# Optimization experiments

Hardware: AMD Instinct MI355X
Metric: run time of the kernel (lower is better)

## Reference

```python
import jax, jax.numpy as jnp
import numpy as np

V = 27      # vocab (26 upper chars + 1)
E = 64      # embedding dim
H = 100     # GRU hidden dim
S = 10      # sequence length
B = 32768   # batch


def setup_inputs() -> dict:
    key = jax.random.key(0)
    ks = jax.random.split(key, 10)
    s = 0.08
    return {
        "encoder_X": jax.random.randint(ks[0], (B, S), 0, V),
        "decoder_X": jax.random.randint(ks[1], (B, S), 0, V),
        "emb": jax.random.normal(ks[2], (V, E)) * s,
        "enc_Wih": jax.random.normal(ks[3], (3 * H, E)) * s,
        "enc_Whh": jax.random.normal(ks[4], (3 * H, H)) * s,
        "enc_bih": jnp.zeros((3 * H,)),
        "enc_bhh": jnp.zeros((3 * H,)),
        "dec_Wih": jax.random.normal(ks[5], (3 * H, E + H)) * s,
        "dec_Whh": jax.random.normal(ks[6], (3 * H, H)) * s,
        "dec_bih": jnp.zeros((3 * H,)),
        "dec_bhh": jnp.zeros((3 * H,)),
        "attn_W": jax.random.normal(ks[7], (H, H)) * s,
        "lin_W": jax.random.normal(ks[8], (V, H)) * s,
        "lin_b": jnp.zeros((V,)),
    }


def gru_cell(x, h, Wih, Whh, bih, bhh):
    # PyTorch GRU cell: gates ordered [reset, update, new]
    gx = x @ Wih.T + bih            # [B, 3H]
    gh = h @ Whh.T + bhh            # [B, 3H]
    xr, xz, xn = jnp.split(gx, 3, axis=-1)
    hr, hz, hn = jnp.split(gh, 3, axis=-1)
    r = jax.nn.sigmoid(xr + hr)
    z = jax.nn.sigmoid(xz + hz)
    n = jnp.tanh(xn + r * hn)
    return (1.0 - z) * n + z * h


def reference(encoder_X, decoder_X, emb, enc_Wih, enc_Whh, enc_bih, enc_bhh,
              dec_Wih, dec_Whh, dec_bih, dec_bhh, attn_W, lin_W, lin_b):
    b = encoder_X.shape[0]
    # ---- encoder ----
    enc_e = emb[encoder_X]                         # [B, S, E]
    h0 = jnp.zeros((b, H), dtype=emb.dtype)

    def enc_step(h, x_t):
        h2 = gru_cell(x_t, h, enc_Wih, enc_Whh, enc_bih, enc_bhh)
        return h2, h2

    hT, enc_seq = jax.lax.scan(enc_step, h0, jnp.swapaxes(enc_e, 0, 1))
    enc_out = jnp.swapaxes(enc_seq, 0, 1)          # [B, S, H]

    # attention_W(encoder_out) is step-invariant: precompute once
    We = enc_out @ attn_W.T                        # [B, S, H]

    # ---- decoder with per-step bilinear attention ----
    dec_e = emb[decoder_X]                         # [B, S, E]

    def dec_step(h, x_t):
        score = jnp.einsum('bsh,bh->bs', We, h)    # [B, S]
        w = jax.nn.softmax(score, axis=1)
        ctx = jnp.einsum('bs,bsh->bh', w, enc_out) # [B, H]
        inp = jnp.concatenate([x_t, ctx], axis=-1) # [B, E+H]
        h2 = gru_cell(inp, h, dec_Wih, dec_Whh, dec_bih, dec_bhh)
        return h2, h2

    _, dec_seq = jax.lax.scan(dec_step, hT, jnp.swapaxes(dec_e, 0, 1))
    dec_out = jnp.swapaxes(dec_seq, 0, 1)          # [B, S, H]

    logits = dec_out @ lin_W.T + lin_b             # [B, S, V]
    return logits.reshape(-1, V)                   # [B*S, V]
```

## Files before the change

kernel.cpp:

```cpp
#include <hip/hip_runtime.h>
#include <hip/hip_bf16.h>

typedef short s16x8 __attribute__((ext_vector_type(8)));
typedef float f32x4 __attribute__((ext_vector_type(4)));
typedef unsigned short ushort_t;
typedef unsigned int uint;

#define DEV static __device__ __forceinline__

namespace {
constexpr int kV = 27, kS = 10, kB = 32768;
constexpr int BT = 32, NB = kB / BT;

constexpr size_t O_BE_R   = 0;
constexpr size_t O_BE_Z   = O_BE_R   + (size_t)7*4*512;
constexpr size_t O_BE_NH  = O_BE_Z   + (size_t)7*4*512;
constexpr size_t O_BE_NHL = O_BE_NH  + (size_t)7*4*512;
constexpr size_t O_BE_NX  = O_BE_NHL + (size_t)7*4*512;
constexpr size_t O_BE_NXL = O_BE_NX  + (size_t)7*1*512;
constexpr size_t O_BD_R   = O_BE_NXL + (size_t)7*1*512;
constexpr size_t O_BD_Z   = O_BD_R   + (size_t)7*8*512;
constexpr size_t O_BD_NC  = O_BD_Z   + (size_t)7*8*512;
constexpr size_t O_BD_NCL = O_BD_NC  + (size_t)7*5*512;
constexpr size_t O_BD_NH  = O_BD_NCL + (size_t)7*5*512;
constexpr size_t O_BD_NHL = O_BD_NH  + (size_t)7*4*512;
constexpr size_t O_WATT   = O_BD_NHL + (size_t)7*4*512;
constexpr size_t O_BLIN   = O_WATT   + (size_t)7*4*512;
constexpr size_t O_BLINL  = O_BLIN   + (size_t)2*4*512;

constexpr int ESTR = 102;
constexpr int EPL  = BT * ESTR;
}

DEV float sigm(float x) { return 1.f / (1.f + __expf(-x)); }
DEV float tanh_(float x) {
  const float ax = fabsf(x), t = __expf(-2.f * ax);
  return copysignf((1.f - t) / (1.f + t), x);
}
DEV ushort_t f2b(float f) { return __builtin_bit_cast(ushort_t, __float2bfloat16(f)); }
DEV float b2f(ushort_t u) { return __builtin_bit_cast(float, (uint)u << 16); }
DEV float lo16(uint u) { return __builtin_bit_cast(float, u << 16); }
DEV float hi16(uint u) { return __builtin_bit_cast(float, u & 0xFFFF0000u); }
DEV f32x4 MF(s16x8 a, s16x8 b, f32x4 c) {
  return __builtin_amdgcn_mfma_f32_16x16x32_bf16(a, b, c, 0, 0, 0);
}
DEV float dot64(const float* __restrict__ a, const float* __restrict__ b) {
  float s = 0.f;
#pragma unroll 16
  for (int k = 0; k < 64; ++k) s += a[k] * b[k];
  return s;
}
DEV void storeHL(ushort_t* ws, size_t offH, size_t offL, int e, float v) {
  const ushort_t h = f2b(v);
  ws[offH + e] = h;
  ws[offL + e] = f2b(v - b2f(h));
}

DEV s16x8 ldBF(const ushort_t* p, int fragIdx, int lane) {
  return __builtin_bit_cast(s16x8, *(const uint4*)(p + ((size_t)fragIdx << 9) + (lane << 3)));
}
DEV uint swzb(int row, int byteoff) { return (uint)((row * 512 + byteoff) ^ ((row & 7) << 4)); }
DEV s16x8 ldA(const ushort_t* A, int rt, int kf, int cl, int g4) {
  const int row = rt * 16 + cl;
  return __builtin_bit_cast(s16x8, *(const uint4*)((const char*)A + swzb(row, kf * 64 + g4 * 16)));
}
DEV void stA16(ushort_t* A, int row, int col, ushort_t v) {
  *(ushort_t*)((char*)A + swzb(row, col * 2)) = v;
}
DEV void stA32(ushort_t* A, int row, int byteoff, uint v) {
  *(uint*)((char*)A + swzb(row, byteoff)) = v;
}
DEV uint ldA32(const ushort_t* A, int row, int byteoff) {
  return *(const uint*)((const char*)A + swzb(row, byteoff));
}

__global__ void seq2seq_setup(const float* __restrict__ emb,
    const float* __restrict__ eWih, const float* __restrict__ eWhh,
    const float* __restrict__ ebih, const float* __restrict__ ebhh,
    const float* __restrict__ dWih, const float* __restrict__ dWhh,
    const float* __restrict__ dbih, const float* __restrict__ dbhh,
    const float* __restrict__ attnW, const float* __restrict__ linW,
    const float* __restrict__ linb, ushort_t* __restrict__ ws) {
  const int t0 = blockIdx.x * blockDim.x + threadIdx.x;
  const int stp = gridDim.x * blockDim.x;

  for (int e = t0; e < 7 * 4 * 512; e += stp) {
    int c = e >> 11, rem = e & 2047, fi = rem >> 9, l = (rem >> 3) & 63, i8 = rem & 7;
    int d = 16 * c + (l & 15);
    int k = fi * 32 + ((l >> 4) << 3) + i8;
    float vr = 0, vz = 0, vnh = 0;
    if (d < 100) {
      if (k < 100) { vr = eWhh[d*100+k]; vz = eWhh[(100+d)*100+k]; vnh = eWhh[(200+d)*100+k]; }
      else if (k < 127) {
        int tok = k - 100;
        vr = dot64(emb + tok*64, eWih + (size_t)d*64);
        vz = dot64(emb + tok*64, eWih + (size_t)(100+d)*64);
      } else {
        vr = ebih[d] + ebhh[d]; vz = ebih[100+d] + ebhh[100+d]; vnh = ebhh[200+d];
      }
    }
    ws[O_BE_R + e] = f2b(vr);
    ws[O_BE_Z + e] = f2b(vz);
    storeHL(ws, O_BE_NH, O_BE_NHL, e, vnh);
  }
  for (int e = t0; e < 7 * 512; e += stp) {
    int c = e >> 9, l = (e >> 3) & 63, i8 = e & 7;
    int d = 16 * c + (l & 15);
    int k = 96 + ((l >> 4) << 3) + i8;
    float v = 0;
    if (d < 100) {
      if (k >= 100 && k < 127) v = dot64(emb + (k-100)*64, eWih + (size_t)(200+d)*64);
      else if (k == 127) v = ebih[200+d];
    }
    storeHL(ws, O_BE_NX, O_BE_NXL, e, v);
  }
  for (int e = t0; e < 7 * 8 * 512; e += stp) {
    int c = e >> 12, rem = e & 4095, fi = rem >> 9, l = (rem >> 3) & 63, i8 = rem & 7;
    int d = 16 * c + (l & 15);
    int k = fi * 32 + ((l >> 4) << 3) + i8;
    float vr = 0, vz = 0;
    if (d < 100) {
      int wr = d, wz = 100 + d;
      if (k < 100)       { vr = dWih[(size_t)wr*164+64+k]; vz = dWih[(size_t)wz*164+64+k]; }
      else if (k < 128)  { }
      else if (k < 228)  { vr = dWhh[wr*100+k-128];        vz = dWhh[wz*100+k-128]; }
      else if (k < 255)  { vr = dot64(emb+(k-228)*64, dWih+(size_t)wr*164);
                           vz = dot64(emb+(k-228)*64, dWih+(size_t)wz*164); }
      else               { vr = dbih[wr]+dbhh[wr];         vz = dbih[wz]+dbhh[wz]; }
    }
    ws[O_BD_R + e] = f2b(vr);
    ws[O_BD_Z + e] = f2b(vz);
  }
  for (int e = t0; e < 7 * 5 * 512; e += stp) {
    int c = e / (5*512), rem = e - c*5*512, fi = rem >> 9, l = (rem >> 3) & 63, i8 = rem & 7;
    int fid = (fi < 4) ? fi : 7;
    int d = 16 * c + (l & 15);
    int k = fid * 32 + ((l >> 4) << 3) + i8;
    float v = 0;
    if (d < 100) {
      int wr = 200 + d;
      if (k < 100) v = dWih[(size_t)wr*164+64+k];
      else if (k >= 228 && k < 255) v = dot64(emb+(k-228)*64, dWih+(size_t)wr*164);
      else if (k == 255) v = dbih[wr];
    }
    storeHL(ws, O_BD_NC, O_BD_NCL, e, v);
  }
  for (int e = t0; e < 7 * 4 * 512; e += stp) {
    int c = e >> 11, rem = e & 2047, fi = rem >> 9, l = (rem >> 3) & 63, i8 = rem & 7;
    int d = 16 * c + (l & 15);
    int k = (4 + fi) * 32 + ((l >> 4) << 3) + i8;
    float v = 0;
    if (d < 100) {
      int wr = 200 + d;
      if (k >= 128 && k < 228) v = dWhh[wr*100+k-128];
      else if (k == 255) v = dbhh[wr];
    }
    storeHL(ws, O_BD_NH, O_BD_NHL, e, v);
  }
  for (int e = t0; e < 7 * 4 * 512; e += stp) {
    int c = e >> 11, rem = e & 2047, fi = rem >> 9, l = (rem >> 3) & 63, i8 = rem & 7;
    int d = 16 * c + (l & 15);
    int k = (4 + fi) * 32 + ((l >> 4) << 3) + i8;
    float v = 0;
    if (d < 100 && k >= 128 && k < 228) v = attnW[(k-128)*100 + d];
    ws[O_WATT + e] = f2b(v);
  }
  for (int e = t0; e < 2 * 4 * 512; e += stp) {
    int c = e >> 11, rem = e & 2047, fi = rem >> 9, l = (rem >> 3) & 63, i8 = rem & 7;
    int vv = 16 * c + (l & 15);
    int k = (4 + fi) * 32 + ((l >> 4) << 3) + i8;
    float v = 0;
    if (vv < kV) {
      if (k >= 128 && k < 228) v = linW[vv*100 + k-128];
      else if (k == 255) v = linb[vv];
    }
    storeHL(ws, O_BLIN, O_BLINL, e, v);
  }
}

__global__ __launch_bounds__(512, 2)
void seq2seq_main(const int* __restrict__ encX, const int* __restrict__ decX,
                  const ushort_t* __restrict__ ws, float* __restrict__ out) {
  const int tid  = threadIdx.x;
  const int lane = tid & 63;
  const int w    = __builtin_amdgcn_readfirstlane(tid >> 6);
  const int cl   = lane & 15, g4 = lane >> 4;
  const int c    = w;
  const int b0   = blockIdx.x * BT;

  __shared__ alignas(16) ushort_t Ash[BT * 256];
  __shared__ alignas(16) ushort_t Esh[kS * EPL];

  const ushort_t* BER   = ws + O_BE_R;
  const ushort_t* BEZ   = ws + O_BE_Z;
  const ushort_t* BENH  = ws + O_BE_NH;
  const ushort_t* BENHL = ws + O_BE_NHL;
  const ushort_t* BENX  = ws + O_BE_NX;
  const ushort_t* BENXL = ws + O_BE_NXL;
  const ushort_t* BDR   = ws + O_BD_R;
  const ushort_t* BDZ   = ws + O_BD_Z;
  const ushort_t* BDNC  = ws + O_BD_NC;
  const ushort_t* BDNCL = ws + O_BD_NCL;
  const ushort_t* BDNH  = ws + O_BD_NH;
  const ushort_t* BDNHL = ws + O_BD_NHL;
  const ushort_t* WATT  = ws + O_WATT;
  const ushort_t* BLIN  = ws + O_BLIN;
  const ushort_t* BLINL = ws + O_BLINL;

  float hreg[2][4];
#pragma unroll
  for (int rt = 0; rt < 2; ++rt)
#pragma unroll
    for (int i = 0; i < 4; ++i) hreg[rt][i] = 0.f;

  auto onehot = [&](const int* X, int tt, int baseByte) {
    if (tid < 128) {
      const int row = tid & 31, grp = tid >> 5;
      const int tok = X[(b0 + row) * kS + tt];
#pragma unroll
      for (int p = 0; p < 4; ++p) {
        const int j0 = grp * 8 + 2 * p;
        if (j0 <= 26) {
          const uint lo = (j0 == tok || j0 == 27) ? 0x3F80u : 0u;
          const uint hi = (j0 + 1 == tok || j0 + 1 == 27) ? 0x3F80u : 0u;
          stA32(Ash, row, baseByte + j0 * 2, lo | (hi << 16));
        }
      }
    }
  };

  for (int i = tid; i < BT * 256 / 2; i += 512) ((uint*)Ash)[i] = 0u;
  __syncthreads();
  onehot(encX, 0, 200);
  __syncthreads();

  for (int t = 0; t < kS; ++t) {
    if (w < 7) {
      f32x4 R[2], Zx[2], NHa[2], NXa[2];
#pragma unroll
      for (int rt = 0; rt < 2; ++rt) {
        R[rt] = f32x4{0,0,0,0}; Zx[rt] = f32x4{0,0,0,0};
        NHa[rt] = f32x4{0,0,0,0}; NXa[rt] = f32x4{0,0,0,0};
      }
#pragma unroll
      for (int kf = 0; kf < 4; ++kf) {
        s16x8 a[2];
#pragma unroll
        for (int rt = 0; rt < 2; ++rt) a[rt] = ldA(Ash, rt, kf, cl, g4);
        s16x8 br  = ldBF(BER,   c * 4 + kf, lane);
        s16x8 bz  = ldBF(BEZ,   c * 4 + kf, lane);
        s16x8 bh  = ldBF(BENH,  c * 4 + kf, lane);
        s16x8 bhl = ldBF(BENHL, c * 4 + kf, lane);
#pragma unroll
        for (int rt = 0; rt < 2; ++rt) {
          R[rt]   = MF(a[rt], br, R[rt]);
          Zx[rt]  = MF(a[rt], bz, Zx[rt]);
          NHa[rt] = MF(a[rt], bh, NHa[rt]);
          NHa[rt] = MF(a[rt], bhl, NHa[rt]);
        }
        if (kf == 3) {
          s16x8 bx  = ldBF(BENX,  c, lane);
          s16x8 bxl = ldBF(BENXL, c, lane);
#pragma unroll
          for (int rt = 0; rt < 2; ++rt) {
            NXa[rt] = MF(a[rt], bx, NXa[rt]);
            NXa[rt] = MF(a[rt], bxl, NXa[rt]);
          }
        }
      }
#pragma unroll
      for (int rt = 0; rt < 2; ++rt)
#pragma unroll
        for (int i = 0; i < 4; ++i) {
          const float r = sigm(R[rt][i]);
          const float z = sigm(Zx[rt][i]);
          const float n = tanh_(NXa[rt][i] + r * NHa[rt][i]);
          hreg[rt][i] = (1.f - z) * n + z * hreg[rt][i];
        }
    }
    __syncthreads();
    if (w < 7) {
      const int d = 16 * c + cl;
      if (d < 100) {
#pragma unroll
        for (int rt = 0; rt < 2; ++rt)
#pragma unroll
          for (int i = 0; i < 4; ++i) {
            const int row = rt * 16 + g4 * 4 + i;
            const ushort_t us = f2b(hreg[rt][i]);
            Esh[t * EPL + row * ESTR + d] = us;
            stA16(Ash, row, (t < 9) ? d : 128 + d, us);
          }
      }
    }
    if (t < 9) onehot(encX, t + 1, 200);
    else       onehot(decX, 0, 456);
    __syncthreads();
  }

  for (int t = 0; t < kS; ++t) {
    if (w < 7) {
      f32x4 G[2] = {f32x4{0,0,0,0}, f32x4{0,0,0,0}};
#pragma unroll
      for (int fi = 0; fi < 4; ++fi) {
        s16x8 bg = ldBF(WATT, c * 4 + fi, lane);
#pragma unroll
        for (int rt = 0; rt < 2; ++rt)
          G[rt] = MF(ldA(Ash, rt, 4 + fi, cl, g4), bg, G[rt]);
      }
      const int d = 16 * c + cl;
      if (d < 100) {
#pragma unroll
        for (int rt = 0; rt < 2; ++rt)
#pragma unroll
          for (int i = 0; i < 4; ++i)
            stA16(Ash, rt * 16 + g4 * 4 + i, d, f2b(G[rt][i]));
      }
    }
    __syncthreads();
    if (w < 5) {
      const int s = 2 * w + (lane >> 5);
      const int r = lane & 31;
      const ushort_t* ep = Esh + s * EPL + r * ESTR;
      float acc = 0.f;
#pragma unroll
      for (int jj = 0; jj < 50; ++jj) {
        const uint gv = ldA32(Ash, r, jj * 4);
        const uint ev = *(const uint*)(ep + jj * 2);
        acc += lo16(gv) * lo16(ev) + hi16(gv) * hi16(ev);
      }
      *(float*)(ep + 100) = acc;
    }
    __syncthreads();
    {
      const int r = lane & 31;
      const int W = w * 2 + (lane >> 5);
      float wat[10];
      {
        float sc[10];
#pragma unroll
        for (int s = 0; s < 10; ++s) sc[s] = *(const float*)(Esh + s * EPL + r * ESTR + 100);
        float m = sc[0];
#pragma unroll
        for (int s = 1; s < 10; ++s) m = fmaxf(m, sc[s]);
        float sum = 0.f;
#pragma unroll
        for (int s = 0; s < 10; ++s) { wat[s] = __expf(sc[s] - m); sum += wat[s]; }
        const float inv = 1.f / sum;
#pragma unroll
        for (int s = 0; s < 10; ++s) wat[s] *= inv;
      }
#pragma unroll
      for (int u = 0; u < 4; ++u) {
        const int j = W * 4 + u;
        if (j < 50) {
          float v0 = 0.f, v1 = 0.f;
#pragma unroll
          for (int s = 0; s < 10; ++s) {
            const uint ev = *(const uint*)(Esh + s * EPL + r * ESTR + 2 * j);
            v0 += wat[s] * lo16(ev);
            v1 += wat[s] * hi16(ev);
          }
          stA32(Ash, r, 4 * j, (uint)f2b(v0) | ((uint)f2b(v1) << 16));
        }
      }
    }
    __syncthreads();
    if (w < 7) {
      f32x4 R[2], Zx[2], NC[2], NHa[2];
#pragma unroll
      for (int rt = 0; rt < 2; ++rt) {
        R[rt] = f32x4{0,0,0,0}; Zx[rt] = f32x4{0,0,0,0};
        NC[rt] = f32x4{0,0,0,0}; NHa[rt] = f32x4{0,0,0,0};
      }
#pragma unroll
      for (int kf = 0; kf < 8; ++kf) {
        s16x8 a[2];
#pragma unroll
        for (int rt = 0; rt < 2; ++rt) a[rt] = ldA(Ash, rt, kf, cl, g4);
        s16x8 br = ldBF(BDR, c * 8 + kf, lane);
        s16x8 bz = ldBF(BDZ, c * 8 + kf, lane);
#pragma unroll
        for (int rt = 0; rt < 2; ++rt) {
          R[rt]  = MF(a[rt], br, R[rt]);
          Zx[rt] = MF(a[rt], bz, Zx[rt]);
        }
        if (kf < 4 || kf == 7) {
          const int fi = (kf < 4) ? kf : 4;
          s16x8 bnc  = ldBF(BDNC,  c * 5 + fi, lane);
          s16x8 bncl = ldBF(BDNCL, c * 5 + fi, lane);
#pragma unroll
          for (int rt = 0; rt < 2; ++rt) {
            NC[rt] = MF(a[rt], bnc, NC[rt]);
            NC[rt] = MF(a[rt], bncl, NC[rt]);
          }
        }
        if (kf >= 4) {
          const int fi = kf - 4;
          s16x8 bnh  = ldBF(BDNH,  c * 4 + fi, lane);
          s16x8 bnhl = ldBF(BDNHL, c * 4 + fi, lane);
#pragma unroll
          for (int rt = 0; rt < 2; ++rt) {
            NHa[rt] = MF(a[rt], bnh, NHa[rt]);
            NHa[rt] = MF(a[rt], bnhl, NHa[rt]);
          }
        }
      }
#pragma unroll
      for (int rt = 0; rt < 2; ++rt)
#pragma unroll
        for (int i = 0; i < 4; ++i) {
          const float r = sigm(R[rt][i]);
          const float z = sigm(Zx[rt][i]);
          const float n = tanh_(NC[rt][i] + r * NHa[rt][i]);
          hreg[rt][i] = (1.f - z) * n + z * hreg[rt][i];
        }
    }
    __syncthreads();
    if (w < 7) {
      const int d = 16 * c + cl;
      if (d < 100) {
#pragma unroll
        for (int rt = 0; rt < 2; ++rt)
#pragma unroll
          for (int i = 0; i < 4; ++i)
            stA16(Ash, rt * 16 + g4 * 4 + i, 128 + d, f2b(hreg[rt][i]));
      }
    }
    if (t < 9) onehot(decX, t + 1, 456);
    __syncthreads();
    if (w < 4) {
      const int rtL = w >> 1, vt = w & 1;
      f32x4 aL = f32x4{0,0,0,0};
#pragma unroll
      for (int fi = 0; fi < 4; ++fi) {
        s16x8 a = ldA(Ash, rtL, 4 + fi, cl, g4);
        aL = MF(a, ldBF(BLIN,  vt * 4 + fi, lane), aL);
        aL = MF(a, ldBF(BLINL, vt * 4 + fi, lane), aL);
      }
      const int v = vt * 16 + cl;
      if (v < kV) {
#pragma unroll
        for (int i = 0; i < 4; ++i) {
          const int row = rtL * 16 + g4 * 4 + i;
          __builtin_nontemporal_store(aL[i], &out[((size_t)(b0 + row) * kS + t) * kV + v]);
        }
      }
    }
  }
}

extern "C" void kernel_launch(void* const* d_in, const int* in_sizes, int n_in,
                              void* d_out, int out_size, void* d_ws, size_t ws_size,
                              hipStream_t stream) {
  const int*   encX = (const int*)d_in[0];
  const int*   decX = (const int*)d_in[1];
  const float* emb  = (const float*)d_in[2];
  const float* eWih = (const float*)d_in[3];
  const float* eWhh = (const float*)d_in[4];
  const float* ebih = (const float*)d_in[5];
  const float* ebhh = (const float*)d_in[6];
  const float* dWih = (const float*)d_in[7];
  const float* dWhh = (const float*)d_in[8];
  const float* dbih = (const float*)d_in[9];
  const float* dbhh = (const float*)d_in[10];
  const float* attW = (const float*)d_in[11];
  const float* linW = (const float*)d_in[12];
  const float* linb = (const float*)d_in[13];
  ushort_t* ws = (ushort_t*)d_ws;
  float* o = (float*)d_out;

  seq2seq_setup<<<128, 256, 0, stream>>>(emb, eWih, eWhh, ebih, ebhh,
                                         dWih, dWhh, dbih, dbhh, attW, linW, linb, ws);
  seq2seq_main<<<NB, 512, 0, stream>>>(encX, decX, ws, o);
}
```

Baseline: 427.9 us.

## Interleave two batch tiles per block to overlap dependent recurrence phases

Each block now handles two 32-row tiles with separate shared buffers and hidden states. The encoder and decoder phases of one tile are staggered against the other, so MFMA work, attention reductions and output projection from different tiles run between the same barriers. This is meant to fill the barrier-separated idle phases where only some waves were busy. In exchange it doubles shared memory and register state per block, which can lower occupancy under launch_bounds(512,2), and it halves the grid size.

New measurement: 447.9 us. +4.7%, slower.

```diff
diff --git a/kernel.cpp b/kernel.cpp
--- a/kernel.cpp
+++ b/kernel.cpp
@@ -10,7 +10,8 @@
 
 namespace {
 constexpr int kV = 27, kS = 10, kB = 32768;
-constexpr int BT = 32, NB = kB / BT;
+constexpr int BT = 32;
+constexpr int NB = kB / (2 * BT);
 
 constexpr size_t O_BE_R   = 0;
 constexpr size_t O_BE_Z   = O_BE_R   + (size_t)7*4*512;
@@ -186,10 +187,12 @@
   const int w    = __builtin_amdgcn_readfirstlane(tid >> 6);
   const int cl   = lane & 15, g4 = lane >> 4;
   const int c    = w;
-  const int b0   = blockIdx.x * BT;
-
-  __shared__ alignas(16) ushort_t Ash[BT * 256];
-  __shared__ alignas(16) ushort_t Esh[kS * EPL];
+  const int b0   = blockIdx.x * (2 * BT);
+
+  __shared__ alignas(16) ushort_t Ash0[BT * 256];
+  __shared__ alignas(16) ushort_t Ash1[BT * 256];
+  __shared__ alignas(16) ushort_t Esh0[kS * EPL];
+  __shared__ alignas(16) ushort_t Esh1[kS * EPL];
 
   const ushort_t* BER   = ws + O_BE_R;
   const ushort_t* BEZ   = ws + O_BE_Z;
@@ -207,78 +210,75 @@
   const ushort_t* BLIN  = ws + O_BLIN;
   const ushort_t* BLINL = ws + O_BLINL;
 
-  float hreg[2][4];
-#pragma unroll
-  for (int rt = 0; rt < 2; ++rt)
-#pragma unroll
-    for (int i = 0; i < 4; ++i) hreg[rt][i] = 0.f;
-
-  auto onehot = [&](const int* X, int tt, int baseByte) {
+  float hreg[2][2][4];
+#pragma unroll
+  for (int tl = 0; tl < 2; ++tl)
+#pragma unroll
+    for (int rt = 0; rt < 2; ++rt)
+#pragma unroll
+      for (int i = 0; i < 4; ++i) hreg[tl][rt][i] = 0.f;
+
+  auto onehot = [&](const int* X, int tt, int baseByte, ushort_t* A, int rowBase) {
     if (tid < 128) {
       const int row = tid & 31, grp = tid >> 5;
-      const int tok = X[(b0 + row) * kS + tt];
+      const int tok = X[(rowBase + row) * kS + tt];
 #pragma unroll
       for (int p = 0; p < 4; ++p) {
         const int j0 = grp * 8 + 2 * p;
         if (j0 <= 26) {
           const uint lo = (j0 == tok || j0 == 27) ? 0x3F80u : 0u;
           const uint hi = (j0 + 1 == tok || j0 + 1 == 27) ? 0x3F80u : 0u;
-          stA32(Ash, row, baseByte + j0 * 2, lo | (hi << 16));
+          stA32(A, row, baseByte + j0 * 2, lo | (hi << 16));
         }
       }
     }
   };
 
-  for (int i = tid; i < BT * 256 / 2; i += 512) ((uint*)Ash)[i] = 0u;
-  __syncthreads();
-  onehot(encX, 0, 200);
-  __syncthreads();
-
-  for (int t = 0; t < kS; ++t) {
-    if (w < 7) {
-      f32x4 R[2], Zx[2], NHa[2], NXa[2];
+  auto E1 = [&](ushort_t* A, float (*hr)[4]) {
+    if (w >= 7) return;
+    f32x4 R[2], Zx[2], NHa[2], NXa[2];
+#pragma unroll
+    for (int rt = 0; rt < 2; ++rt) {
+      R[rt] = f32x4{0,0,0,0}; Zx[rt] = f32x4{0,0,0,0};
+      NHa[rt] = f32x4{0,0,0,0}; NXa[rt] = f32x4{0,0,0,0};
+    }
+#pragma unroll
+    for (int kf = 0; kf < 4; ++kf) {
+      s16x8 a[2];
+#pragma unroll
+      for (int rt = 0; rt < 2; ++rt) a[rt] = ldA(A, rt, kf, cl, g4);
+      s16x8 br  = ldBF(BER,   c * 4 + kf, lane);
+      s16x8 bz  = ldBF(BEZ,   c * 4 + kf, lane);
+      s16x8 bh  = ldBF(BENH,  c * 4 + kf, lane);
+      s16x8 bhl = ldBF(BENHL, c * 4 + kf, lane);
 #pragma unroll
       for (int rt = 0; rt < 2; ++rt) {
-        R[rt] = f32x4{0,0,0,0}; Zx[rt] = f32x4{0,0,0,0};
-        NHa[rt] = f32x4{0,0,0,0}; NXa[rt] = f32x4{0,0,0,0};
-      }
-#pragma unroll
-      for (int kf = 0; kf < 4; ++kf) {
-        s16x8 a[2];
-#pragma unroll
-        for (int rt = 0; rt < 2; ++rt) a[rt] = ldA(Ash, rt, kf, cl, g4);
-        s16x8 br  = ldBF(BER,   c * 4 + kf, lane);
-        s16x8 bz  = ldBF(BEZ,   c * 4 + kf, lane);
-        s16x8 bh  = ldBF(BENH,  c * 4 + kf, lane);
-        s16x8 bhl = ldBF(BENHL, c * 4 + kf, lane);
+        R[rt]   = MF(a[rt], br, R[rt]);
+        Zx[rt]  = MF(a[rt], bz, Zx[rt]);
+        NHa[rt] = MF(a[rt], bh, NHa[rt]);
+        NHa[rt] = MF(a[rt], bhl, NHa[rt]);
+      }
+      if (kf == 3) {
+        s16x8 bx  = ldBF(BENX,  c, lane);
+        s16x8 bxl = ldBF(BENXL, c, lane);
 #pragma unroll
         for (int rt = 0; rt < 2; ++rt) {
-          R[rt]   = MF(a[rt], br, R[rt]);
-          Zx[rt]  = MF(a[rt], bz, Zx[rt]);
-          NHa[rt] = MF(a[rt], bh, NHa[rt]);
-          NHa[rt] = MF(a[rt], bhl, NHa[rt]);
+          NXa[rt] = MF(a[rt], bx, NXa[rt]);
+          NXa[rt] = MF(a[rt], bxl, NXa[rt]);
         }
-        if (kf == 3) {
-          s16x8 bx  = ldBF(BENX,  c, lane);
-          s16x8 bxl = ldBF(BENXL, c, lane);
-#pragma unroll
-          for (int rt = 0; rt < 2; ++rt) {
-            NXa[rt] = MF(a[rt], bx, NXa[rt]);
-            NXa[rt] = MF(a[rt], bxl, NXa[rt]);
-          }
-        }
-      }
-#pragma unroll
-      for (int rt = 0; rt < 2; ++rt)
-#pragma unroll
-        for (int i = 0; i < 4; ++i) {
-          const float r = sigm(R[rt][i]);
-          const float z = sigm(Zx[rt][i]);
-          const float n = tanh_(NXa[rt][i] + r * NHa[rt][i]);
-          hreg[rt][i] = (1.f - z) * n + z * hreg[rt][i];
-        }
-    }
-    __syncthreads();
+      }
+    }
+#pragma unroll
+    for (int rt = 0; rt < 2; ++rt)
+#pragma unroll
+      for (int i = 0; i < 4; ++i) {
+        const float r = sigm(R[rt][i]);
+        const float z = sigm(Zx[rt][i]);
+        const float n = tanh_(NXa[rt][i] + r * NHa[rt][i]);
+        hr[rt][i] = (1.f - z) * n + z * hr[rt][i];
+      }
+  };
+  auto E2 = [&](ushort_t* A, ushort_t* E, float (*hr)[4], int t, int rowBase) {
     if (w < 7) {
       const int d = 16 * c + cl;
       if (d < 100) {
@@ -287,136 +287,134 @@
 #pragma unroll
           for (int i = 0; i < 4; ++i) {
             const int row = rt * 16 + g4 * 4 + i;
-            const ushort_t us = f2b(hreg[rt][i]);
-            Esh[t * EPL + row * ESTR + d] = us;
-            stA16(Ash, row, (t < 9) ? d : 128 + d, us);
+            const ushort_t us = f2b(hr[rt][i]);
+            E[t * EPL + row * ESTR + d] = us;
+            stA16(A, row, (t < 9) ? d : 128 + d, us);
           }
       }
     }
-    if (t < 9) onehot(encX, t + 1, 200);
-    else       onehot(decX, 0, 456);
-    __syncthreads();
-  }
-
-  for (int t = 0; t < kS; ++t) {
-    if (w < 7) {
-      f32x4 G[2] = {f32x4{0,0,0,0}, f32x4{0,0,0,0}};
-#pragma unroll
-      for (int fi = 0; fi < 4; ++fi) {
-        s16x8 bg = ldBF(WATT, c * 4 + fi, lane);
-#pragma unroll
-        for (int rt = 0; rt < 2; ++rt)
-          G[rt] = MF(ldA(Ash, rt, 4 + fi, cl, g4), bg, G[rt]);
-      }
-      const int d = 16 * c + cl;
-      if (d < 100) {
-#pragma unroll
-        for (int rt = 0; rt < 2; ++rt)
-#pragma unroll
-          for (int i = 0; i < 4; ++i)
-            stA16(Ash, rt * 16 + g4 * 4 + i, d, f2b(G[rt][i]));
-      }
-    }
-    __syncthreads();
-    if (w < 5) {
-      const int s = 2 * w + (lane >> 5);
-      const int r = lane & 31;
-      const ushort_t* ep = Esh + s * EPL + r * ESTR;
-      float acc = 0.f;
-#pragma unroll
-      for (int jj = 0; jj < 50; ++jj) {
-        const uint gv = ldA32(Ash, r, jj * 4);
-        const uint ev = *(const uint*)(ep + jj * 2);
-        acc += lo16(gv) * lo16(ev) + hi16(gv) * hi16(ev);
-      }
-      *(float*)(ep + 100) = acc;
-    }
-    __syncthreads();
+    if (t < 9) onehot(encX, t + 1, 200, A, rowBase);
+    else       onehot(decX, 0, 456, A, rowBase);
+  };
+
+  auto D1 = [&](ushort_t* A) {
+    if (w >= 7) return;
+    f32x4 G[2] = {f32x4{0,0,0,0}, f32x4{0,0,0,0}};
+#pragma unroll
+    for (int fi = 0; fi < 4; ++fi) {
+      s16x8 bg = ldBF(WATT, c * 4 + fi, lane);
+#pragma unroll
+      for (int rt = 0; rt < 2; ++rt)
+        G[rt] = MF(ldA(A, rt, 4 + fi, cl, g4), bg, G[rt]);
+    }
+    const int d = 16 * c + cl;
+    if (d < 100) {
+#pragma unroll
+      for (int rt = 0; rt < 2; ++rt)
+#pragma unroll
+        for (int i = 0; i < 4; ++i)
+          stA16(A, rt * 16 + g4 * 4 + i, d, f2b(G[rt][i]));
+    }
+  };
+  auto D2 = [&](ushort_t* A, ushort_t* E) {
+    if (w >= 5) return;
+    const int s = 2 * w + (lane >> 5);
+    const int r = lane & 31;
+    ushort_t* ep = E + s * EPL + r * ESTR;
+    float acc = 0.f;
+#pragma unroll
+    for (int jj = 0; jj < 50; ++jj) {
+      const uint gv = ldA32(A, r, jj * 4);
+      const uint ev = *(const uint*)(ep + jj * 2);
+      acc += lo16(gv) * lo16(ev) + hi16(gv) * hi16(ev);
+    }
+    *(float*)(ep + 100) = acc;
+  };
+  auto D3 = [&](ushort_t* A, ushort_t* E) {
+    const int r = lane & 31;
+    const int W = w * 2 + (lane >> 5);
+    float wat[10];
     {
-      const int r = lane & 31;
-      const int W = w * 2 + (lane >> 5);
-      float wat[10];
-      {
-        float sc[10];
-#pragma unroll
-        for (int s = 0; s < 10; ++s) sc[s] = *(const float*)(Esh + s * EPL + r * ESTR + 100);
-        float m = sc[0];
-#pragma unroll
-        for (int s = 1; s < 10; ++s) m = fmaxf(m, sc[s]);
-        float sum = 0.f;
-#pragma unroll
-        for (int s = 0; s < 10; ++s) { wat[s] = __expf(sc[s] - m); sum += wat[s]; }
-        const float inv = 1.f / sum;
-#pragma unroll
-        for (int s = 0; s < 10; ++s) wat[s] *= inv;
-      }
-#pragma unroll
-      for (int u = 0; u < 4; ++u) {
-        const int j = W * 4 + u;
-        if (j < 50) {
-          float v0 = 0.f, v1 = 0.f;
-#pragma unroll
-          for (int s = 0; s < 10; ++s) {
-            const uint ev = *(const uint*)(Esh + s * EPL + r * ESTR + 2 * j);
-            v0 += wat[s] * lo16(ev);
-            v1 += wat[s] * hi16(ev);
-          }
-          stA32(Ash, r, 4 * j, (uint)f2b(v0) | ((uint)f2b(v1) << 16));
+      float sc[10];
+#pragma unroll
+      for (int s = 0; s < 10; ++s) sc[s] = *(const float*)(E + s * EPL + r * ESTR + 100);
+      float m = sc[0];
+#pragma unroll
+      for (int s = 1; s < 10; ++s) m = fmaxf(m, sc[s]);
+      float sum = 0.f;
+#pragma unroll
+      for (int s = 0; s < 10; ++s) { wat[s] = __expf(sc[s] - m); sum += wat[s]; }
+      const float inv = 1.f / sum;
+#pragma unroll
+      for (int s = 0; s < 10; ++s) wat[s] *= inv;
+    }
+#pragma unroll
+    for (int u = 0; u < 4; ++u) {
+      const int j = W * 4 + u;
+      if (j < 50) {
+        float v0 = 0.f, v1 = 0.f;
+#pragma unroll
+        for (int s = 0; s < 10; ++s) {
+          const uint ev = *(const uint*)(E + s * EPL + r * ESTR + 2 * j);
+          v0 += wat[s] * lo16(ev);
+          v1 += wat[s] * hi16(ev);
         }
-      }
-    }
-    __syncthreads();
-    if (w < 7) {
-      f32x4 R[2], Zx[2], NC[2], NHa[2];
+        stA32(A, r, 4 * j, (uint)f2b(v0) | ((uint)f2b(v1) << 16));
+      }
+    }
+  };
+  auto D4 = [&](ushort_t* A, float (*hr)[4]) {
+    if (w >= 7) return;
+    f32x4 R[2], Zx[2], NC[2], NHa[2];
+#pragma unroll
+    for (int rt = 0; rt < 2; ++rt) {
+      R[rt] = f32x4{0,0,0,0}; Zx[rt] = f32x4{0,0,0,0};
+      NC[rt] = f32x4{0,0,0,0}; NHa[rt] = f32x4{0,0,0,0};
+    }
+#pragma unroll
+    for (int kf = 0; kf < 8; ++kf) {
+      s16x8 a[2];
+#pragma unroll
+      for (int rt = 0; rt < 2; ++rt) a[rt] = ldA(A, rt, kf, cl, g4);
+      s16x8 br = ldBF(BDR, c * 8 + kf, lane);
+      s16x8 bz = ldBF(BDZ, c * 8 + kf, lane);
 #pragma unroll
       for (int rt = 0; rt < 2; ++rt) {
-        R[rt] = f32x4{0,0,0,0}; Zx[rt] = f32x4{0,0,0,0};
-        NC[rt] = f32x4{0,0,0,0}; NHa[rt] = f32x4{0,0,0,0};
-      }
-#pragma unroll
-      for (int kf = 0; kf < 8; ++kf) {
-        s16x8 a[2];
-#pragma unroll
-        for (int rt = 0; rt < 2; ++rt) a[rt] = ldA(Ash, rt, kf, cl, g4);
-        s16x8 br = ldBF(BDR, c * 8 + kf, lane);
-        s16x8 bz = ldBF(BDZ, c * 8 + kf, lane);
+        R[rt]  = MF(a[rt], br, R[rt]);
+        Zx[rt] = MF(a[rt], bz, Zx[rt]);
+      }
+      if (kf < 4 || kf == 7) {
+        const int fi = (kf < 4) ? kf : 4;
+        s16x8 bnc  = ldBF(BDNC,  c * 5 + fi, lane);
+        s16x8 bncl = ldBF(BDNCL, c * 5 + fi, lane);
 #pragma unroll
         for (int rt = 0; rt < 2; ++rt) {
-          R[rt]  = MF(a[rt], br, R[rt]);
-          Zx[rt] = MF(a[rt], bz, Zx[rt]);
+          NC[rt] = MF(a[rt], bnc, NC[rt]);
+          NC[rt] = MF(a[rt], bncl, NC[rt]);
         }
-        if (kf < 4 || kf == 7) {
-          const int fi = (kf < 4) ? kf : 4;
-          s16x8 bnc  = ldBF(BDNC,  c * 5 + fi, lane);
-          s16x8 bncl = ldBF(BDNCL, c * 5 + fi, lane);
-#pragma unroll
-          for (int rt = 0; rt < 2; ++rt) {
-            NC[rt] = MF(a[rt], bnc, NC[rt]);
-            NC[rt] = MF(a[rt], bncl, NC[rt]);
-          }
+      }
+      if (kf >= 4) {
+        const int fi = kf - 4;
+        s16x8 bnh  = ldBF(BDNH,  c * 4 + fi, lane);
+        s16x8 bnhl = ldBF(BDNHL, c * 4 + fi, lane);
+#pragma unroll
+        for (int rt = 0; rt < 2; ++rt) {
+          NHa[rt] = MF(a[rt], bnh, NHa[rt]);
+          NHa[rt] = MF(a[rt], bnhl, NHa[rt]);
         }
-        if (kf >= 4) {
-          const int fi = kf - 4;
-          s16x8 bnh  = ldBF(BDNH,  c * 4 + fi, lane);
-          s16x8 bnhl = ldBF(BDNHL, c * 4 + fi, lane);
-#pragma unroll
-          for (int rt = 0; rt < 2; ++rt) {
-            NHa[rt] = MF(a[rt], bnh, NHa[rt]);
-            NHa[rt] = MF(a[rt], bnhl, NHa[rt]);
-          }
-        }
-      }
-#pragma unroll
-      for (int rt = 0; rt < 2; ++rt)
-#pragma unroll
-        for (int i = 0; i < 4; ++i) {
-          const float r = sigm(R[rt][i]);
-          const float z = sigm(Zx[rt][i]);
-          const float n = tanh_(NC[rt][i] + r * NHa[rt][i]);
-          hreg[rt][i] = (1.f - z) * n + z * hreg[rt][i];
-        }
-    }
-    __syncthreads();
+      }
+    }
+#pragma unroll
+    for (int rt = 0; rt < 2; ++rt)
+#pragma unroll
+      for (int i = 0; i < 4; ++i) {
+        const float r = sigm(R[rt][i]);
+        const float z = sigm(Zx[rt][i]);
+        const float n = tanh_(NC[rt][i] + r * NHa[rt][i]);
+        hr[rt][i] = (1.f - z) * n + z * hr[rt][i];
+      }
+  };
+  auto D5 = [&](ushort_t* A, float (*hr)[4], int t, int rowBase) {
     if (w < 7) {
       const int d = 16 * c + cl;
       if (d < 100) {
@@ -424,30 +422,77 @@
         for (int rt = 0; rt < 2; ++rt)
 #pragma unroll
           for (int i = 0; i < 4; ++i)
-            stA16(Ash, rt * 16 + g4 * 4 + i, 128 + d, f2b(hreg[rt][i]));
-      }
-    }
-    if (t < 9) onehot(decX, t + 1, 456);
-    __syncthreads();
-    if (w < 4) {
-      const int rtL = w >> 1, vt = w & 1;
-      f32x4 aL = f32x4{0,0,0,0};
-#pragma unroll
-      for (int fi = 0; fi < 4; ++fi) {
-        s16x8 a = ldA(Ash, rtL, 4 + fi, cl, g4);
-        aL = MF(a, ldBF(BLIN,  vt * 4 + fi, lane), aL);
-        aL = MF(a, ldBF(BLINL, vt * 4 + fi, lane), aL);
-      }
-      const int v = vt * 16 + cl;
-      if (v < kV) {
-#pragma unroll
-        for (int i = 0; i < 4; ++i) {
-          const int row = rtL * 16 + g4 * 4 + i;
-          __builtin_nontemporal_store(aL[i], &out[((size_t)(b0 + row) * kS + t) * kV + v]);
-        }
-      }
-    }
-  }
+            stA16(A, rt * 16 + g4 * 4 + i, 128 + d, f2b(hr[rt][i]));
+      }
+    }
+    if (t < 9) onehot(decX, t + 1, 456, A, rowBase);
+  };
+  auto D6 = [&](ushort_t* A, int t, int rowBase) {
+    if (w >= 4) return;
+    const int rtL = w >> 1, vt = w & 1;
+    f32x4 aL = f32x4{0,0,0,0};
+#pragma unroll
+    for (int fi = 0; fi < 4; ++fi) {
+      s16x8 a = ldA(A, rtL, 4 + fi, cl, g4);
+      aL = MF(a, ldBF(BLIN,  vt * 4 + fi, lane), aL);
+      aL = MF(a, ldBF(BLINL, vt * 4 + fi, lane), aL);
+    }
+    const int v = vt * 16 + cl;
+    if (v < kV) {
+#pragma unroll
+      for (int i = 0; i < 4; ++i) {
+        const int row = rtL * 16 + g4 * 4 + i;
+        __builtin_nontemporal_store(aL[i], &out[((size_t)(rowBase + row) * kS + t) * kV + v]);
+      }
+    }
+  };
+
+  for (int i = tid; i < BT * 256 / 2; i += 512) { ((uint*)Ash0)[i] = 0u; ((uint*)Ash1)[i] = 0u; }
+  __syncthreads();
+  onehot(encX, 0, 200, Ash0, b0);
+  onehot(encX, 0, 200, Ash1, b0 + BT);
+  __syncthreads();
+
+  E1(Ash0, hreg[0]);
+  __syncthreads();
+  E2(Ash0, Esh0, hreg[0], 0, b0); E1(Ash1, hreg[1]);
+  __syncthreads();
+#pragma unroll 1
+  for (int t = 1; t < kS; ++t) {
+    E1(Ash0, hreg[0]); E2(Ash1, Esh1, hreg[1], t - 1, b0 + BT);
+    __syncthreads();
+    E2(Ash0, Esh0, hreg[0], t, b0); E1(Ash1, hreg[1]);
+    __syncthreads();
+  }
+  E2(Ash1, Esh1, hreg[1], 9, b0 + BT);
+  __syncthreads();
+
+#pragma unroll 1
+  for (int t = 0; t < kS; ++t) {
+    if (t) D6(Ash0, t - 1, b0);
+    D1(Ash0);
+    if (t) D4(Ash1, hreg[1]);
+    __syncthreads();
+    D2(Ash0, Esh0);
+    if (t) D5(Ash1, hreg[1], t - 1, b0 + BT);
+    __syncthreads();
+    D3(Ash0, Esh0);
+    if (t) D6(Ash1, t - 1, b0 + BT);
+    D1(Ash1);
+    __syncthreads();
+    D4(Ash0, hreg[0]);
+    D2(Ash1, Esh1);
+    __syncthreads();
+    D5(Ash0, hreg[0], t, b0);
+    D3(Ash1, Esh1);
+    __syncthreads();
+  }
+  D6(Ash0, 9, b0);
+  D4(Ash1, hreg[1]);
+  __syncthreads();
+  D5(Ash1, hreg[1], 9, b0 + BT);
+  __syncthreads();
+  D6(Ash1, 9, b0 + BT);
 }
 
 extern "C" void kernel_launch(void* const* d_in, const int* in_sizes, int n_in,
```

## Fuse attention score and context into one phase with 16-lane shuffle reductions

Applied to the files above, without the earlier changes.

The attention scores are now computed by all 8 waves, with each group of 16 lanes splitting one row's 100-element dot product and reducing through xor shuffles, instead of 5 waves each doing a serial 50-iteration loop per row. That removes the score round-trip through shared memory and one block-wide barrier per decoder step. The context computation is remapped to the same row and lane layout. The time-step loops are also marked not to unroll and the weight pointers are inlined, probably to limit register pressure and code size, at the cost of some extra shuffle instructions.

New measurement: 430.3 us. Within noise of the previous version (+0.6%).

```diff
diff --git a/kernel.cpp b/kernel.cpp
--- a/kernel.cpp
+++ b/kernel.cpp
@@ -191,19 +191,6 @@
   __shared__ alignas(16) ushort_t Ash[BT * 256];
   __shared__ alignas(16) ushort_t Esh[kS * EPL];
 
-  const ushort_t* BER   = ws + O_BE_R;
-  const ushort_t* BEZ   = ws + O_BE_Z;
-  const ushort_t* BENH  = ws + O_BE_NH;
-  const ushort_t* BENHL = ws + O_BE_NHL;
-  const ushort_t* BENX  = ws + O_BE_NX;
-  const ushort_t* BENXL = ws + O_BE_NXL;
-  const ushort_t* BDR   = ws + O_BD_R;
-  const ushort_t* BDZ   = ws + O_BD_Z;
-  const ushort_t* BDNC  = ws + O_BD_NC;
-  const ushort_t* BDNCL = ws + O_BD_NCL;
-  const ushort_t* BDNH  = ws + O_BD_NH;
-  const ushort_t* BDNHL = ws + O_BD_NHL;
-  const ushort_t* WATT  = ws + O_WATT;
   const ushort_t* BLIN  = ws + O_BLIN;
   const ushort_t* BLINL = ws + O_BLINL;
 
@@ -234,6 +221,7 @@
   onehot(encX, 0, 200);
   __syncthreads();
 
+#pragma unroll 1
   for (int t = 0; t < kS; ++t) {
     if (w < 7) {
       f32x4 R[2], Zx[2], NHa[2], NXa[2];
@@ -247,10 +235,10 @@
         s16x8 a[2];
 #pragma unroll
         for (int rt = 0; rt < 2; ++rt) a[rt] = ldA(Ash, rt, kf, cl, g4);
-        s16x8 br  = ldBF(BER,   c * 4 + kf, lane);
-        s16x8 bz  = ldBF(BEZ,   c * 4 + kf, lane);
-        s16x8 bh  = ldBF(BENH,  c * 4 + kf, lane);
-        s16x8 bhl = ldBF(BENHL, c * 4 + kf, lane);
+        s16x8 br  = ldBF(ws + O_BE_R,   c * 4 + kf, lane);
+        s16x8 bz  = ldBF(ws + O_BE_Z,   c * 4 + kf, lane);
+        s16x8 bh  = ldBF(ws + O_BE_NH,  c * 4 + kf, lane);
+        s16x8 bhl = ldBF(ws + O_BE_NHL, c * 4 + kf, lane);
 #pragma unroll
         for (int rt = 0; rt < 2; ++rt) {
           R[rt]   = MF(a[rt], br, R[rt]);
@@ -259,8 +247,8 @@
           NHa[rt] = MF(a[rt], bhl, NHa[rt]);
         }
         if (kf == 3) {
-          s16x8 bx  = ldBF(BENX,  c, lane);
-          s16x8 bxl = ldBF(BENXL, c, lane);
+          s16x8 bx  = ldBF(ws + O_BE_NX,  c, lane);
+          s16x8 bxl = ldBF(ws + O_BE_NXL, c, lane);
 #pragma unroll
           for (int rt = 0; rt < 2; ++rt) {
             NXa[rt] = MF(a[rt], bx, NXa[rt]);
@@ -298,12 +286,13 @@
     __syncthreads();
   }
 
+#pragma unroll 1
   for (int t = 0; t < kS; ++t) {
     if (w < 7) {
       f32x4 G[2] = {f32x4{0,0,0,0}, f32x4{0,0,0,0}};
 #pragma unroll
       for (int fi = 0; fi < 4; ++fi) {
-        s16x8 bg = ldBF(WATT, c * 4 + fi, lane);
+        s16x8 bg = ldBF(ws + O_WATT, c * 4 + fi, lane);
 #pragma unroll
         for (int rt = 0; rt < 2; ++rt)
           G[rt] = MF(ldA(Ash, rt, 4 + fi, cl, g4), bg, G[rt]);
@@ -318,28 +307,35 @@
       }
     }
     __syncthreads();
-    if (w < 5) {
-      const int s = 2 * w + (lane >> 5);
-      const int r = lane & 31;
-      const ushort_t* ep = Esh + s * EPL + r * ESTR;
-      float acc = 0.f;
-#pragma unroll
-      for (int jj = 0; jj < 50; ++jj) {
-        const uint gv = ldA32(Ash, r, jj * 4);
-        const uint ev = *(const uint*)(ep + jj * 2);
-        acc += lo16(gv) * lo16(ev) + hi16(gv) * hi16(ev);
-      }
-      *(float*)(ep + 100) = acc;
-    }
-    __syncthreads();
     {
-      const int r = lane & 31;
-      const int W = w * 2 + (lane >> 5);
+      const int r  = 4 * w + g4;
+      const int j  = cl;
+      const int nidx = (j < 2) ? 4 : 3;
+      uint gvv[4];
+#pragma unroll
+      for (int u = 0; u < 4; ++u)
+        gvv[u] = (u < nidx) ? ldA32(Ash, r, 4 * (j + 16 * u)) : 0u;
+
+      float sc[10];
+#pragma unroll
+      for (int s = 0; s < 10; ++s) {
+        const ushort_t* ep = Esh + s * EPL + r * ESTR;
+        float acc = 0.f;
+#pragma unroll
+        for (int u = 0; u < 4; ++u) {
+          if (u < nidx) {
+            const uint ev = *(const uint*)(ep + 2 * (j + 16 * u));
+            acc += lo16(gvv[u]) * lo16(ev) + hi16(gvv[u]) * hi16(ev);
+          }
+        }
+        acc += __shfl_xor(acc, 1);
+        acc += __shfl_xor(acc, 2);
+        acc += __shfl_xor(acc, 4);
+        acc += __shfl_xor(acc, 8);
+        sc[s] = acc;
+      }
       float wat[10];
       {
-        float sc[10];
-#pragma unroll
-        for (int s = 0; s < 10; ++s) sc[s] = *(const float*)(Esh + s * EPL + r * ESTR + 100);
         float m = sc[0];
 #pragma unroll
         for (int s = 1; s < 10; ++s) m = fmaxf(m, sc[s]);
@@ -352,16 +348,16 @@
       }
 #pragma unroll
       for (int u = 0; u < 4; ++u) {
-        const int j = W * 4 + u;
-        if (j < 50) {
+        if (u < nidx) {
+          const int idx = j + 16 * u;
           float v0 = 0.f, v1 = 0.f;
 #pragma unroll
           for (int s = 0; s < 10; ++s) {
-            const uint ev = *(const uint*)(Esh + s * EPL + r * ESTR + 2 * j);
+            const uint ev = *(const uint*)(Esh + s * EPL + r * ESTR + 2 * idx);
             v0 += wat[s] * lo16(ev);
             v1 += wat[s] * hi16(ev);
           }
-          stA32(Ash, r, 4 * j, (uint)f2b(v0) | ((uint)f2b(v1) << 16));
+          stA32(Ash, r, 4 * idx, (uint)f2b(v0) | ((uint)f2b(v1) << 16));
         }
       }
     }
@@ -378,8 +374,8 @@
         s16x8 a[2];
 #pragma unroll
         for (int rt = 0; rt < 2; ++rt) a[rt] = ldA(Ash, rt, kf, cl, g4);
-        s16x8 br = ldBF(BDR, c * 8 + kf, lane);
-        s16x8 bz = ldBF(BDZ, c * 8 + kf, lane);
+        s16x8 br = ldBF(ws + O_BD_R, c * 8 + kf, lane);
+        s16x8 bz = ldBF(ws + O_BD_Z, c * 8 + kf, lane);
 #pragma unroll
         for (int rt = 0; rt < 2; ++rt) {
           R[rt]  = MF(a[rt], br, R[rt]);
@@ -387,8 +383,8 @@
         }
         if (kf < 4 || kf == 7) {
           const int fi = (kf < 4) ? kf : 4;
-          s16x8 bnc  = ldBF(BDNC,  c * 5 + fi, lane);
-          s16x8 bncl = ldBF(BDNCL, c * 5 + fi, lane);
+          s16x8 bnc  = ldBF(ws + O_BD_NC,  c * 5 + fi, lane);
+          s16x8 bncl = ldBF(ws + O_BD_NCL, c * 5 + fi, lane);
 #pragma unroll
           for (int rt = 0; rt < 2; ++rt) {
             NC[rt] = MF(a[rt], bnc, NC[rt]);
@@ -397,8 +393,8 @@
         }
         if (kf >= 4) {
           const int fi = kf - 4;
-          s16x8 bnh  = ldBF(BDNH,  c * 4 + fi, lane);
-          s16x8 bnhl = ldBF(BDNHL, c * 4 + fi, lane);
+          s16x8 bnh  = ldBF(ws + O_BD_NH,  c * 4 + fi, lane);
+          s16x8 bnhl = ldBF(ws + O_BD_NHL, c * 4 + fi, lane);
 #pragma unroll
           for (int rt = 0; rt < 2; ++rt) {
             NHa[rt] = MF(a[rt], bnh, NHa[rt]);
```
